# Performance work log

Measured on AMD Instinct MI355X. Metric: run time of the kernel, lower is better.

## Reference

```python
import jax, jax.numpy as jnp
import numpy as np

TAU = 2.0
V_TH = 0.5
BN_EPS = 1e-5
ALPHA = 2.0  # spikingjelly surrogate.ATan default

@jax.custom_vjp
def spike_fn(x):
    # Heaviside forward, ATan surrogate backward (defined for fwdbwd parity)
    return (x >= 0.0).astype(x.dtype)

def _spike_fwd(x):
    return spike_fn(x), x

def _spike_bwd(x, g):
    return (g * (ALPHA / 2.0) / (1.0 + (jnp.pi / 2.0 * ALPHA * x) ** 2),)

spike_fn.defvjp(_spike_fwd, _spike_bwd)

def lif_multistep(x_seq):
    # MultiStepLIFNode: v <- v + (x - v)/tau ; spike = H(v - v_th) ; hard reset v<-v*(1-sg(spike))
    def step(v, x_t):
        v = v + (x_t - v) / TAU
        s = spike_fn(v - V_TH)
        v = v * (1.0 - jax.lax.stop_gradient(s))  # detach_reset=True, v_reset=0
        return v, s
    v0 = jnp.zeros_like(x_seq[0])
    _, spikes = jax.lax.scan(step, v0, x_seq)
    return spikes

def setup_inputs() -> dict:
    key = jax.random.key(0)
    k1, k2, k3 = jax.random.split(key, 3)
    T, B, N, D = 4, 64, 256, 512
    x = jax.random.normal(k1, (T, B, N, D), jnp.float32)
    mx = jax.random.normal(k2, (N, B, T, D), jnp.float32)
    W = jax.random.normal(k3, (D, D), jnp.float32) / np.sqrt(D).astype(np.float32)
    gamma = jnp.ones((D,), jnp.float32)
    beta = jnp.zeros((D,), jnp.float32)
    return {"x": x, "mx": mx, "W": W, "gamma": gamma, "beta": beta}

def reference(x, mx, W, gamma, beta):
    # mx: [N,B,T,D] -> transpose(0,2) -> [T,B,N,D]
    mxt = jnp.transpose(mx, (2, 1, 0, 3))
    # Linear (no bias): [T,B,N,D] @ W^T
    h = jnp.einsum('tbnd,ed->tbne', mxt, W)
    # BatchNorm1d(D) in training mode: stats over (T*B, N) per channel D (biased var)
    mean = h.mean(axis=(0, 1, 2))
    var = h.var(axis=(0, 1, 2))
    hn = (h - mean) * jax.lax.rsqrt(var + BN_EPS) * gamma + beta
    # LIF recurrence over T
    s = lif_multistep(hn)  # [T,B,N,D] binary spikes
    return x * s
```

## Files before the change

### kernel.cpp

```cpp
#include <hip/hip_runtime.h>
#include <math.h>

namespace {
constexpr int TDIM = 4, BDIM = 64, NDIM = 256, DDIM = 512;
constexpr int MROWS = 65536;
constexpr long long BND = 8388608LL;
constexpr double BN_EPS = 1e-5;

constexpr int BM = 64, BNT = 128, BK = 32;
constexpr int APITCH = BK + 2;
constexpr int WPITCH = BNT + 4;
constexpr int LDS_BYTES = (BM * APITCH + BK * WPITCH) * 8;

constexpr int BM3 = 128, BN3 = 64, BK3 = 16;
constexpr int AP3 = BM3 + 1;
constexpr int WP3 = BN3 + 1;

constexpr int NSA = 6, NSW = 5;
constexpr long long APL = 33554432LL;
constexpr long long WPL = 262144LL;
constexpr int CH8 = 22528;
}

typedef double d4 __attribute__((ext_vector_type(4)));
typedef int i32x4 __attribute__((ext_vector_type(4)));
typedef int i32x16 __attribute__((ext_vector_type(16)));

#define GLOAD16(g, d) __builtin_amdgcn_global_load_lds( \
    (const __attribute__((address_space(1))) void*)(g), \
    (__attribute__((address_space(3))) void*)(d), 16, 0, 0)

__global__ void probe_k(double* __restrict__ rowmap)
{
    const int l = threadIdx.x;
    d4 z = {0.0, 0.0, 0.0, 0.0};
    d4 dr = __builtin_amdgcn_mfma_f64_16x16x4f64((double)(l & 15), 1.0, z, 0, 0, 0);
#pragma unroll
    for (int r = 0; r < 4; ++r)
        rowmap[l * 4 + r] = dr[r] * 0.25;
}

__global__ void probe8_k(double* __restrict__ irow8, double* __restrict__ icol8)
{
    const int l = threadIdx.x;
    i32x16 z;
#pragma unroll
    for (int r = 0; r < 16; ++r) z[r] = 0;
    const int mb = (l & 31) * 0x01010101;
    const int ob = 0x01010101;
    i32x4 am = {mb, mb, mb, mb};
    i32x4 a1 = {ob, ob, ob, ob};
    i32x16 d1 = __builtin_amdgcn_mfma_i32_32x32x32_i8(am, a1, z, 0, 0, 0);
#pragma unroll
    for (int r = 0; r < 16; ++r)
        irow8[l * 16 + r] = (double)d1[r] / 32.0;
    i32x16 d2 = __builtin_amdgcn_mfma_i32_32x32x32_i8(a1, am, z, 0, 0, 0);
    icol8[l] = (double)d2[0] / 32.0;
}

__global__ __launch_bounds__(256)
void slice_a_k(const float* __restrict__ src, char* __restrict__ dst)
{
    const int ri  = threadIdx.x & 63;
    const int ks0 = threadIdx.x >> 6;
    const long long row = (long long)blockIdx.x * 64 + ri;
#pragma unroll 1
    for (int it = 0; it < 8; ++it) {
        const int kseg = it * 4 + ks0;
        const float* sp = src + row * DDIM + kseg * 16;
        union { char c[16]; i32x4 v; } pk[NSA];
#pragma unroll
        for (int e = 0; e < 16; ++e) {
            const double V = (double)sp[e] * 4.0;
            const double u = rint(V);
            pk[0].c[e] = (char)(int)u;
            float r = (float)(V - u);
#pragma unroll
            for (int s = 1; s < NSA; ++s) {
                r *= 128.0f;
                const float uf = rintf(r);
                r -= uf;
                pk[s].c[e] = (char)(int)uf;
            }
        }
        const long long base = (long long)blockIdx.x * 32768 + kseg * 1024 + ri * 16;
#pragma unroll
        for (int s = 0; s < NSA; ++s)
            *(i32x4*)(dst + (long long)s * APL + base) = pk[s].v;
    }
}

__global__ __launch_bounds__(256)
void slice_w_k(const float* __restrict__ src, char* __restrict__ dst)
{
    const int cbk  = blockIdx.x >> 3;
    const int kgrp = blockIdx.x & 7;
    const int ci   = threadIdx.x & 63;
    const int kseg = kgrp * 4 + (threadIdx.x >> 6);
    const float* sp = src + (long long)(cbk * 64 + ci) * DDIM + kseg * 16;
    union { char c[16]; i32x4 v; } pk[NSW];
#pragma unroll
    for (int e = 0; e < 16; ++e) {
        const double V = (double)sp[e] * 256.0;
        const double u = rint(V);
        pk[0].c[e] = (char)(int)u;
        float r = (float)(V - u);
#pragma unroll
        for (int s = 1; s < NSW; ++s) {
            r *= 128.0f;
            const float uf = rintf(r);
            r -= uf;
            pk[s].c[e] = (char)(int)uf;
        }
    }
    const long long base = (long long)cbk * 32768 + kseg * 1024 + ci * 16;
#pragma unroll
    for (int s = 0; s < NSW; ++s)
        *(i32x4*)(dst + (long long)s * WPL + base) = pk[s].v;
}

template<int NW>
struct Stager {
    const char* gb[NW];
    int lo[NW];
    __device__ __forceinline__ void init(int w0, const char* Asl, const char* Wsl,
                                         long long aT, long long wT, int l)
    {
#pragma unroll
        for (int i = 0; i < NW; ++i) {
            const int idx = w0 + i;
            if (idx < 12) {
                gb[i] = Asl + (long long)(idx >> 1) * APL + aT
                      + (long long)(idx & 1) * 1024 + l * 16;
                lo[i] = (idx >> 1) * 2048 + (idx & 1) * 1024;
            } else {
                const int e = idx - 12;
                gb[i] = Wsl + (long long)(e >> 1) * WPL + wT
                      + (long long)(e & 1) * 1024 + l * 16;
                lo[i] = 12288 + (e >> 1) * 2048 + (e & 1) * 1024;
            }
        }
    }
    __device__ __forceinline__ void issue(char* buf, int ck)
    {
        const int go = ck * 2048;
#pragma unroll
        for (int i = 0; i < NW; ++i)
            GLOAD16(gb[i] + go, buf + lo[i]);
    }
};

template<int NW>
__device__ __forceinline__ void gemm8_loop(Stager<NW>& st, char* smb,
                                           i32x16 (&acc)[6], int roA, int roW,
                                           int c0)
{
#pragma unroll 2
    for (int c = 0; c < 16; ++c) {
        const char* bA = smb + (c & 1) * CH8;
        const char* bW = bA + 12288;
        i32x4 af[NSA], wf[NSW];
#pragma unroll
        for (int s = 0; s < NSA; ++s)
            af[s] = *(const i32x4*)(bA + s * 2048 + roA);
#pragma unroll
        for (int t = 0; t < NSW; ++t)
            wf[t] = *(const i32x4*)(bW + t * 2048 + roW);
#pragma unroll
        for (int s = 0; s < NSA; ++s)
#pragma unroll
            for (int t = 0; t < NSW; ++t)
                if (s + t <= 5)
                    acc[s + t] = __builtin_amdgcn_mfma_i32_32x32x32_i8(
                                     af[s], wf[t], acc[s + t], 0, 0, 0);
        if (c == 15) break;
        asm volatile("s_barrier" ::: "memory");
        if (c < 14) {
            st.issue(smb + (c & 1) * CH8, (c0 + c + 2) & 15);
            if constexpr (NW == 6)
                asm volatile("s_waitcnt vmcnt(6)" ::: "memory");
            else
                asm volatile("s_waitcnt vmcnt(5)" ::: "memory");
        } else {
            asm volatile("s_waitcnt vmcnt(0)" ::: "memory");
        }
        __builtin_amdgcn_sched_barrier(0);
        asm volatile("s_barrier" ::: "memory");
        __builtin_amdgcn_sched_barrier(0);
    }
}

__global__ __launch_bounds__(256, 3)
void gemm8_k(const char* __restrict__ Asl, const char* __restrict__ Wsl,
             double* __restrict__ hbuf, double* __restrict__ sums,
             const double* __restrict__ irow8, const double* __restrict__ icol8)
{
    __shared__ __align__(16) char sm[2][CH8];

    const int tid = threadIdx.x;
    const int bid = blockIdx.x;
    const int rb  = ((bid >> 6) << 3) | (bid & 7);
    const int cb  = (bid >> 3) & 7;

    const int c0 = (((bid >> 6) * 5) + ((bid & 7) * 3)) & 15;

    const int w  = tid >> 6;
    const int l  = tid & 63;
    const int wr = w >> 1;
    const int wc = w & 1;

    const long long aTile = (long long)rb * 32768;
    const long long wTile = (long long)cb * 32768;

    i32x16 acc[6];
#pragma unroll
    for (int g = 0; g < 6; ++g)
#pragma unroll
        for (int r = 0; r < 16; ++r) acc[g][r] = 0;

    const int roA = (l >> 5) * 1024 + (32 * wr + (l & 31)) * 16;
    const int roW = (l >> 5) * 1024 + (32 * wc + (l & 31)) * 16;

    char* smb = &sm[0][0];
    if (w < 2) {
        Stager<6> st;
        st.init(6 * w, Asl, Wsl, aTile, wTile, l);
        st.issue(smb, c0);
        st.issue(smb + CH8, (c0 + 1) & 15);
        asm volatile("s_waitcnt vmcnt(6)" ::: "memory");
        __builtin_amdgcn_sched_barrier(0);
        asm volatile("s_barrier" ::: "memory");
        __builtin_amdgcn_sched_barrier(0);
        gemm8_loop<6>(st, smb, acc, roA, roW, c0);
    } else {
        Stager<5> st;
        st.init(12 + 5 * (w - 2), Asl, Wsl, aTile, wTile, l);
        st.issue(smb, c0);
        st.issue(smb + CH8, (c0 + 1) & 15);
        asm volatile("s_waitcnt vmcnt(5)" ::: "memory");
        __builtin_amdgcn_sched_barrier(0);
        asm volatile("s_barrier" ::: "memory");
        __builtin_amdgcn_sched_barrier(0);
        gemm8_loop<5>(st, smb, acc, roA, roW, c0);
    }

    int irw[16];
#pragma unroll
    for (int r = 0; r < 16; ++r) irw[r] = (int)irow8[l * 16 + r];
    const int icl = (int)icol8[l];

    const double C7 = 1.0 / 128.0, CMB = 1.0 / 1024.0;
    double lsum = 0.0, lsq = 0.0;
    const int colg = cb * 64 + 32 * wc + icl;
    const int row0 = rb * 64 + 32 * wr;
#pragma unroll
    for (int r = 0; r < 16; ++r) {
        double t = (double)acc[5][r];
        t = fma(t, C7, (double)acc[4][r]);
        t = fma(t, C7, (double)acc[3][r]);
        t = fma(t, C7, (double)acc[2][r]);
        t = fma(t, C7, (double)acc[1][r]);
        t = fma(t, C7, (double)acc[0][r]);
        const double h = t * CMB;
        hbuf[(size_t)(row0 + irw[r]) * DDIM + colg] = h;
        lsum += h;
        lsq = fma(h, h, lsq);
    }

    __syncthreads();
    double* Ss = (double*)sm;
    const int ctr = wr * 2 + (l >> 5);
    const int cloc = 32 * wc + icl;
    Ss[cloc * 4 + ctr] = lsum;
    Ss[256 + cloc * 4 + ctr] = lsq;
    __syncthreads();
    if (tid < 64) {
        double s = 0.0, q = 0.0;
#pragma unroll
        for (int k = 0; k < 4; ++k) {
            s += Ss[tid * 4 + k];
            q += Ss[256 + tid * 4 + k];
        }
        atomicAdd(&sums[cb * 64 + tid], s);
        atomicAdd(&sums[512 + cb * 64 + tid], q);
    }
}

__global__ __launch_bounds__(256, 2)
void gemm3_k(const float* __restrict__ mx, const float* __restrict__ Wm,
             double* __restrict__ hbuf, double* __restrict__ sums,
             const double* __restrict__ rowmap)
{
    __shared__ double Atr[BK3 * AP3];
    __shared__ double Wt [BK3 * WP3];

    const int tid = threadIdx.x;
    const int bid = blockIdx.x;
    const int rb  = ((bid >> 6) << 3) | (bid & 7);
    const int cb  = (bid >> 3) & 7;
    const int row0 = rb * BM3;
    const int col0 = cb * BN3;

    const int w  = tid >> 6;
    const int l  = tid & 63;
    const int wr = w >> 1;
    const int wc = w & 1;
    const int lr = l & 15;
    const int kq = l >> 4;

    int irow[4];
#pragma unroll
    for (int r = 0; r < 4; ++r)
        irow[r] = (int)rowmap[l * 4 + r];

    const int arow = tid >> 1;
    const int af   = (tid & 1) * 8;
    const int wrow = tid >> 2;
    const int wf   = (tid & 3) * 4;
    const float* aSrc = mx + (size_t)(row0 + arow) * DDIM + af;
    const float* wSrc = Wm + (size_t)(col0 + wrow) * DDIM + wf;

    d4 acc[4][2];
#pragma unroll
    for (int i = 0; i < 4; ++i)
#pragma unroll
        for (int j = 0; j < 2; ++j) acc[i][j] = (d4){0.0, 0.0, 0.0, 0.0};

    float4 pa0 = *(const float4*)(aSrc + 0);
    float4 pa1 = *(const float4*)(aSrc + 4);
    float4 pw  = *(const float4*)(wSrc + 0);

    for (int kk = 0; kk < DDIM; kk += BK3) {
        __syncthreads();
        Atr[(af + 0) * AP3 + arow] = (double)pa0.x;
        Atr[(af + 1) * AP3 + arow] = (double)pa0.y;
        Atr[(af + 2) * AP3 + arow] = (double)pa0.z;
        Atr[(af + 3) * AP3 + arow] = (double)pa0.w;
        Atr[(af + 4) * AP3 + arow] = (double)pa1.x;
        Atr[(af + 5) * AP3 + arow] = (double)pa1.y;
        Atr[(af + 6) * AP3 + arow] = (double)pa1.z;
        Atr[(af + 7) * AP3 + arow] = (double)pa1.w;
        Wt[(wf + 0) * WP3 + wrow] = (double)pw.x;
        Wt[(wf + 1) * WP3 + wrow] = (double)pw.y;
        Wt[(wf + 2) * WP3 + wrow] = (double)pw.z;
        Wt[(wf + 3) * WP3 + wrow] = (double)pw.w;
        __syncthreads();

        if (kk + BK3 < DDIM) {
            pa0 = *(const float4*)(aSrc + kk + BK3 + 0);
            pa1 = *(const float4*)(aSrc + kk + BK3 + 4);
            pw  = *(const float4*)(wSrc + kk + BK3 + 0);
        }

#pragma unroll
        for (int ks = 0; ks < BK3 / 4; ++ks) {
            const int kabs = ks * 4 + kq;
            double a[4], b[2];
#pragma unroll
            for (int i = 0; i < 4; ++i)
                a[i] = Atr[kabs * AP3 + 64 * wr + 16 * i + lr];
#pragma unroll
            for (int j = 0; j < 2; ++j)
                b[j] = Wt[kabs * WP3 + 32 * wc + 16 * j + lr];
#pragma unroll
            for (int i = 0; i < 4; ++i)
#pragma unroll
                for (int j = 0; j < 2; ++j)
                    acc[i][j] = __builtin_amdgcn_mfma_f64_16x16x4f64(
                                    a[i], b[j], acc[i][j], 0, 0, 0);
        }
    }

#pragma unroll
    for (int i = 0; i < 4; ++i) {
#pragma unroll
        for (int j = 0; j < 2; ++j) {
            const size_t cbase = (size_t)col0 + 32 * wc + 16 * j + lr;
            const size_t rbase = (size_t)row0 + 64 * wr + 16 * i;
#pragma unroll
            for (int r = 0; r < 4; ++r)
                hbuf[(rbase + irow[r]) * DDIM + cbase] = acc[i][j][r];
        }
    }

    __syncthreads();
    double* Ssum = Atr;
    double* Ssq  = Atr + 512;
    const int ctr = wr * 4 + kq;
#pragma unroll
    for (int j = 0; j < 2; ++j) {
        const int cloc = 32 * wc + 16 * j + lr;
        double s = 0.0, q = 0.0;
#pragma unroll
        for (int i = 0; i < 4; ++i)
#pragma unroll
            for (int r = 0; r < 4; ++r) {
                const double v = acc[i][j][r];
                s += v;
                q = fma(v, v, q);
            }
        Ssum[cloc * 8 + ctr] = s;
        Ssq [cloc * 8 + ctr] = q;
    }
    __syncthreads();
    if (tid < 64) {
        double s = 0.0, q = 0.0;
#pragma unroll
        for (int c = 0; c < 8; ++c) {
            s += Ssum[tid * 8 + c];
            q += Ssq [tid * 8 + c];
        }
        atomicAdd(&sums[col0 + tid], s);
        atomicAdd(&sums[512 + col0 + tid], q);
    }
}

template<int MODE>
__global__ __launch_bounds__(256)
void gemm_k(const float* __restrict__ mx, const float* __restrict__ Wm,
            double* __restrict__ hbuf, double* __restrict__ sums,
            const double* __restrict__ scale, const double* __restrict__ shiftv,
            const float* __restrict__ x, float* __restrict__ out)
{
    __shared__ __align__(16) char smem[LDS_BYTES];
    double (*Ald)[APITCH] = reinterpret_cast<double(*)[APITCH]>(smem);
    double (*Wld)[WPITCH] = reinterpret_cast<double(*)[WPITCH]>(smem + (size_t)BM * APITCH * 8);

    const int tid  = threadIdx.x;
    const int rb   = blockIdx.x >> 2;
    const int cb   = blockIdx.x & 3;
    const int row0 = rb * BM;
    const int col0 = cb * BNT;

    const int arow = tid >> 2;
    const int ak   = (tid & 3) * 8;
    const int erow = tid >> 1;
    const int wk   = (tid & 1) * 16;

    const float* aSrc = mx + (size_t)(row0 + arow) * DDIM;
    const float* wSrc = Wm + (size_t)(col0 + erow) * DDIM;

    const int rg = tid >> 4;
    const int cg = tid & 15;

    double acc[4][8];
#pragma unroll
    for (int i = 0; i < 4; ++i)
#pragma unroll
        for (int j = 0; j < 8; ++j) acc[i][j] = 0.0;

    for (int kk = 0; kk < DDIM; kk += BK) {
        const float4 a0 = *(const float4*)(aSrc + kk + ak);
        const float4 a1 = *(const float4*)(aSrc + kk + ak + 4);
        const float4 w0 = *(const float4*)(wSrc + kk + wk);
        const float4 w1 = *(const float4*)(wSrc + kk + wk + 4);
        const float4 w2 = *(const float4*)(wSrc + kk + wk + 8);
        const float4 w3 = *(const float4*)(wSrc + kk + wk + 12);
        __syncthreads();
        Ald[arow][ak + 0] = (double)a0.x; Ald[arow][ak + 1] = (double)a0.y;
        Ald[arow][ak + 2] = (double)a0.z; Ald[arow][ak + 3] = (double)a0.w;
        Ald[arow][ak + 4] = (double)a1.x; Ald[arow][ak + 5] = (double)a1.y;
        Ald[arow][ak + 6] = (double)a1.z; Ald[arow][ak + 7] = (double)a1.w;
        const float wfv[16] = {w0.x, w0.y, w0.z, w0.w, w1.x, w1.y, w1.z, w1.w,
                               w2.x, w2.y, w2.z, w2.w, w3.x, w3.y, w3.z, w3.w};
#pragma unroll
        for (int q = 0; q < 16; ++q) Wld[wk + q][erow] = (double)wfv[q];
        __syncthreads();

#pragma unroll 4
        for (int d = 0; d < BK; ++d) {
            double a[4], wv[8];
#pragma unroll
            for (int i = 0; i < 4; ++i) a[i] = Ald[rg * 4 + i][d];
#pragma unroll
            for (int j = 0; j < 8; ++j) wv[j] = Wld[d][cg * 8 + j];
#pragma unroll
            for (int i = 0; i < 4; ++i)
#pragma unroll
                for (int j = 0; j < 8; ++j)
                    acc[i][j] = fma(a[i], wv[j], acc[i][j]);
        }
    }

    if (MODE <= 1) {
        __syncthreads();
        double* scr = reinterpret_cast<double*>(smem);
#pragma unroll
        for (int j = 0; j < 8; ++j) {
            const double s = acc[0][j] + acc[1][j] + acc[2][j] + acc[3][j];
            const double q = acc[0][j]*acc[0][j] + acc[1][j]*acc[1][j]
                           + acc[2][j]*acc[2][j] + acc[3][j]*acc[3][j];
            scr[(cg * 8 + j) * 16 + rg] = s;
            scr[2048 + (cg * 8 + j) * 16 + rg] = q;
        }
        __syncthreads();
        if (tid < 128) {
            double s = 0.0, q = 0.0;
#pragma unroll
            for (int r = 0; r < 16; ++r) {
                s += scr[tid * 16 + r];
                q += scr[2048 + tid * 16 + r];
            }
            atomicAdd(&sums[col0 + tid], s);
            atomicAdd(&sums[512 + col0 + tid], q);
        }
    }

    if (MODE == 2) {
        const int p  = rb * 16 + rg;
        const int nn = p >> 6;
        const int bb = p & 63;
#pragma unroll
        for (int j = 0; j < 8; ++j) {
            const int e = col0 + cg * 8 + j;
            const double sc = scale[e];
            const double sh = shiftv[e];
            const size_t basex = (size_t)bb * (NDIM * DDIM) + (size_t)nn * DDIM + e;
            double v = 0.0;
#pragma unroll
            for (int t = 0; t < 4; ++t) {
                const double hn = fma(acc[t][j], sc, sh);
                v = v + (hn - v) / 2.0;
                const bool s = (v - 0.5) >= 0.0;
                const size_t xi = (size_t)t * BND + basex;
                out[xi] = s ? x[xi] : 0.0f;
                if (s) v = 0.0;
            }
        }
    }
}

__global__ void zero_k(double* sums)
{
    const int i = blockIdx.x * 256 + threadIdx.x;
    if (i < 1024) sums[i] = 0.0;
}

__global__ void stat_k(const double* __restrict__ sums,
                       const float* __restrict__ gamma, const float* __restrict__ beta,
                       double* __restrict__ scale, double* __restrict__ shiftv)
{
    const int e = blockIdx.x * 256 + threadIdx.x;
    if (e < 512) {
        const double mean = sums[e] * (1.0 / 65536.0);
        const double msq  = sums[512 + e] * (1.0 / 65536.0);
        const double var  = msq - mean * mean;
        const double inv  = 1.0 / sqrt(var + BN_EPS);
        const double g    = (double)gamma[e] * inv;
        scale[e]  = g;
        shiftv[e] = (double)beta[e] - mean * g;
    }
}

__global__ __launch_bounds__(256)
void lifh_k(const double* __restrict__ hbuf, const double* __restrict__ scale,
            const double* __restrict__ shiftv, const float* __restrict__ x,
            float* __restrict__ out)
{
    const size_t i = (size_t)blockIdx.x * 256 + threadIdx.x;
    const int e2 = (int)(i & 255) * 2;
    const size_t p = i >> 8;
    const int nn = (int)(p >> 6);
    const int bb = (int)(p & 63);
    const double2 sc = *(const double2*)&scale[e2];
    const double2 sh = *(const double2*)&shiftv[e2];
    const double* hp = hbuf + p * 2048 + e2;
    const size_t basex = (size_t)bb * (NDIM * DDIM) + (size_t)nn * DDIM + e2;
    double v0 = 0.0, v1 = 0.0;
#pragma unroll
    for (int t = 0; t < 4; ++t) {
        const double2 h2 = *(const double2*)(hp + (size_t)t * 512);
        const double hn0 = fma(h2.x, sc.x, sh.x);
        const double hn1 = fma(h2.y, sc.y, sh.y);
        v0 = v0 + (hn0 - v0) / 2.0;
        v1 = v1 + (hn1 - v1) / 2.0;
        const bool s0 = (v0 - 0.5) >= 0.0;
        const bool s1 = (v1 - 0.5) >= 0.0;
        const size_t xi = (size_t)t * BND + basex;
        const float2 xv = *(const float2*)(x + xi);
        float2 ov;
        ov.x = s0 ? xv.x : 0.0f;
        ov.y = s1 ? xv.y : 0.0f;
        *(float2*)(out + xi) = ov;
        if (s0) v0 = 0.0;
        if (s1) v1 = 0.0;
    }
}

extern "C" void kernel_launch(void* const* d_in, const int* in_sizes, int n_in,
                              void* d_out, int out_size, void* d_ws, size_t ws_size,
                              hipStream_t stream)
{
    const float* x     = (const float*)d_in[0];
    const float* mx    = (const float*)d_in[1];
    const float* Wm    = (const float*)d_in[2];
    const float* gamma = (const float*)d_in[3];
    const float* beta  = (const float*)d_in[4];
    float* out = (float*)d_out;

    char* ws = (char*)d_ws;
    double* sums   = (double*)ws;
    double* scale  = (double*)(ws + 8192);
    double* shiftv = scale + 512;
    double* rowmap = (double*)(ws + 16384);
    double* irow8  = (double*)(ws + 18432);
    double* icol8  = (double*)(ws + 26624);
    double* hbuf   = (double*)(ws + 32768);

    const size_t HBSZ   = (size_t)MROWS * DDIM * 8;
    const size_t OFF_AS = 32768 + HBSZ;
    const size_t ASSZ   = (size_t)NSA * APL;
    const size_t OFF_WS = OFF_AS + ASSZ;
    const size_t WSSZ   = (size_t)NSW * WPL;
    const size_t need8  = OFF_WS + WSSZ;
    const size_t need_h = 32768 + HBSZ;

    hipLaunchKernelGGL(zero_k, dim3(4), dim3(256), 0, stream, sums);

    if (ws_size >= need8) {
        char* Asl = ws + OFF_AS;
        char* Wsl = ws + OFF_WS;
        hipLaunchKernelGGL(probe8_k, dim3(1), dim3(64), 0, stream, irow8, icol8);
        hipLaunchKernelGGL(slice_a_k, dim3(1024), dim3(256), 0, stream, mx, Asl);
        hipLaunchKernelGGL(slice_w_k, dim3(64), dim3(256), 0, stream, Wm, Wsl);
        hipLaunchKernelGGL(gemm8_k, dim3(8192), dim3(256), 0, stream,
                           Asl, Wsl, hbuf, sums, irow8, icol8);
        hipLaunchKernelGGL(stat_k, dim3(2), dim3(256), 0, stream,
                           sums, gamma, beta, scale, shiftv);
        hipLaunchKernelGGL(lifh_k, dim3(16384), dim3(256), 0, stream,
                           hbuf, scale, shiftv, x, out);
    } else if (ws_size >= need_h) {
        hipLaunchKernelGGL(probe_k, dim3(1), dim3(64), 0, stream, rowmap);
        hipLaunchKernelGGL(gemm3_k, dim3(4096), dim3(256), 0, stream,
                           mx, Wm, hbuf, sums, rowmap);
        hipLaunchKernelGGL(stat_k, dim3(2), dim3(256), 0, stream,
                           sums, gamma, beta, scale, shiftv);
        hipLaunchKernelGGL(lifh_k, dim3(16384), dim3(256), 0, stream,
                           hbuf, scale, shiftv, x, out);
    } else {
        hipLaunchKernelGGL((gemm_k<0>), dim3(4096), dim3(256), 0, stream,
                           mx, Wm, nullptr, sums, nullptr, nullptr, nullptr, nullptr);
        hipLaunchKernelGGL(stat_k, dim3(2), dim3(256), 0, stream,
                           sums, gamma, beta, scale, shiftv);
        hipLaunchKernelGGL((gemm_k<2>), dim3(4096), dim3(256), 0, stream,
                           mx, Wm, nullptr, nullptr, scale, shiftv, x, out);
    }
}
```

Before: 472.9 us.

## Restructure int8 GEMM tiles: per-wave private A staging and register-held W fragments

Reworks the int8 sliced GEMM kernel so each block covers 128 rows by 32 columns, and each wave owns a private 32-row A slice. That slice is double-buffered in LDS through direct global-to-LDS loads, while the W fragments go straight into registers. Because no wave reads another wave's LDS data, the two block-wide barriers per K-chunk are dropped. In exchange, W fragments are reloaded from global memory by every wave and there is more register pressure, so launch bounds drop from 3 to 2 blocks per CU. The grid mapping and the BN statistics reduction change to match the new tile shape.

```diff
diff --git a/kernel.cpp b/kernel.cpp
--- a/kernel.cpp
+++ b/kernel.cpp
@@ -19,7 +19,6 @@
 constexpr int NSA = 6, NSW = 5;
 constexpr long long APL = 33554432LL;
 constexpr long long WPL = 262144LL;
-constexpr int CH8 = 22528;
 }
 
 typedef double d4 __attribute__((ext_vector_type(4)));
@@ -119,129 +118,85 @@
         *(i32x4*)(dst + (long long)s * WPL + base) = pk[s].v;
 }
 
-template<int NW>
-struct Stager {
-    const char* gb[NW];
-    int lo[NW];
-    __device__ __forceinline__ void init(int w0, const char* Asl, const char* Wsl,
-                                         long long aT, long long wT, int l)
-    {
-#pragma unroll
-        for (int i = 0; i < NW; ++i) {
-            const int idx = w0 + i;
-            if (idx < 12) {
-                gb[i] = Asl + (long long)(idx >> 1) * APL + aT
-                      + (long long)(idx & 1) * 1024 + l * 16;
-                lo[i] = (idx >> 1) * 2048 + (idx & 1) * 1024;
-            } else {
-                const int e = idx - 12;
-                gb[i] = Wsl + (long long)(e >> 1) * WPL + wT
-                      + (long long)(e & 1) * 1024 + l * 16;
-                lo[i] = 12288 + (e >> 1) * 2048 + (e & 1) * 1024;
-            }
-        }
-    }
-    __device__ __forceinline__ void issue(char* buf, int ck)
-    {
-        const int go = ck * 2048;
-#pragma unroll
-        for (int i = 0; i < NW; ++i)
-            GLOAD16(gb[i] + go, buf + lo[i]);
-    }
-};
-
-template<int NW>
-__device__ __forceinline__ void gemm8_loop(Stager<NW>& st, char* smb,
-                                           i32x16 (&acc)[6], int roA, int roW,
-                                           int c0)
-{
-#pragma unroll 2
-    for (int c = 0; c < 16; ++c) {
-        const char* bA = smb + (c & 1) * CH8;
-        const char* bW = bA + 12288;
-        i32x4 af[NSA], wf[NSW];
-#pragma unroll
-        for (int s = 0; s < NSA; ++s)
-            af[s] = *(const i32x4*)(bA + s * 2048 + roA);
-#pragma unroll
-        for (int t = 0; t < NSW; ++t)
-            wf[t] = *(const i32x4*)(bW + t * 2048 + roW);
-#pragma unroll
-        for (int s = 0; s < NSA; ++s)
-#pragma unroll
-            for (int t = 0; t < NSW; ++t)
-                if (s + t <= 5)
-                    acc[s + t] = __builtin_amdgcn_mfma_i32_32x32x32_i8(
-                                     af[s], wf[t], acc[s + t], 0, 0, 0);
-        if (c == 15) break;
-        asm volatile("s_barrier" ::: "memory");
-        if (c < 14) {
-            st.issue(smb + (c & 1) * CH8, (c0 + c + 2) & 15);
-            if constexpr (NW == 6)
-                asm volatile("s_waitcnt vmcnt(6)" ::: "memory");
-            else
-                asm volatile("s_waitcnt vmcnt(5)" ::: "memory");
-        } else {
-            asm volatile("s_waitcnt vmcnt(0)" ::: "memory");
-        }
-        __builtin_amdgcn_sched_barrier(0);
-        asm volatile("s_barrier" ::: "memory");
-        __builtin_amdgcn_sched_barrier(0);
-    }
-}
-
-__global__ __launch_bounds__(256, 3)
+__global__ __launch_bounds__(256, 2)
 void gemm8_k(const char* __restrict__ Asl, const char* __restrict__ Wsl,
              double* __restrict__ hbuf, double* __restrict__ sums,
              const double* __restrict__ irow8, const double* __restrict__ icol8)
 {
-    __shared__ __align__(16) char sm[2][CH8];
+    __shared__ __align__(16) char sm[49152];
 
     const int tid = threadIdx.x;
     const int bid = blockIdx.x;
-    const int rb  = ((bid >> 6) << 3) | (bid & 7);
-    const int cb  = (bid >> 3) & 7;
-
-    const int c0 = (((bid >> 6) * 5) + ((bid & 7) * 3)) & 15;
-
-    const int w  = tid >> 6;
-    const int l  = tid & 63;
-    const int wr = w >> 1;
-    const int wc = w & 1;
-
-    const long long aTile = (long long)rb * 32768;
-    const long long wTile = (long long)cb * 32768;
+    const int g   = bid >> 7;
+    const int cbb = (bid >> 3) & 15;
+    const int xcd = bid & 7;
+    const int rb  = g * 8 + xcd;
+    const int c0  = ((g * 5) + (cbb * 3)) & 15;
+
+    const int w = tid >> 6;
+    const int l = tid & 63;
+
+    const long long aBase = ((long long)(rb * 2 + (w >> 1))) * 32768
+                          + (long long)(l >> 5) * 1024
+                          + (long long)(32 * (w & 1) + (l & 31)) * 16;
+    const long long wBase = ((long long)(cbb >> 1)) * 32768
+                          + (long long)(l >> 5) * 1024
+                          + (long long)(32 * (cbb & 1) + (l & 31)) * 16;
+
+    char* myA = sm + w * 12288;
 
     i32x16 acc[6];
 #pragma unroll
-    for (int g = 0; g < 6; ++g)
-#pragma unroll
-        for (int r = 0; r < 16; ++r) acc[g][r] = 0;
-
-    const int roA = (l >> 5) * 1024 + (32 * wr + (l & 31)) * 16;
-    const int roW = (l >> 5) * 1024 + (32 * wc + (l & 31)) * 16;
-
-    char* smb = &sm[0][0];
-    if (w < 2) {
-        Stager<6> st;
-        st.init(6 * w, Asl, Wsl, aTile, wTile, l);
-        st.issue(smb, c0);
-        st.issue(smb + CH8, (c0 + 1) & 15);
-        asm volatile("s_waitcnt vmcnt(6)" ::: "memory");
+    for (int gg = 0; gg < 6; ++gg)
+#pragma unroll
+        for (int r = 0; r < 16; ++r) acc[gg][r] = 0;
+
+    i32x4 wreg[2][5];
+
+    {
+        const long long wo = wBase + (long long)c0 * 2048;
+#pragma unroll
+        for (int t = 0; t < 5; ++t)
+            wreg[0][t] = *(const i32x4*)(Wsl + (long long)t * WPL + wo);
+        const long long ao = aBase + (long long)c0 * 2048;
+#pragma unroll
+        for (int s = 0; s < 6; ++s)
+            GLOAD16(Asl + (long long)s * APL + ao, myA + s * 1024);
+    }
+
+#pragma unroll 2
+    for (int c = 0; c < 16; ++c) {
+        const int cur = c & 1;
+        if (c < 15) {
+            const int ck = (c0 + c + 1) & 15;
+            const long long wo = wBase + (long long)ck * 2048;
+#pragma unroll
+            for (int t = 0; t < 5; ++t)
+                wreg[cur ^ 1][t] = *(const i32x4*)(Wsl + (long long)t * WPL + wo);
+            const long long ao = aBase + (long long)ck * 2048;
+#pragma unroll
+            for (int s = 0; s < 6; ++s)
+                GLOAD16(Asl + (long long)s * APL + ao,
+                        myA + (cur ^ 1) * 6144 + s * 1024);
+            __builtin_amdgcn_sched_barrier(0);
+            asm volatile("s_waitcnt vmcnt(11)" ::: "memory");
+        } else {
+            __builtin_amdgcn_sched_barrier(0);
+            asm volatile("s_waitcnt vmcnt(0)" ::: "memory");
+        }
         __builtin_amdgcn_sched_barrier(0);
-        asm volatile("s_barrier" ::: "memory");
-        __builtin_amdgcn_sched_barrier(0);
-        gemm8_loop<6>(st, smb, acc, roA, roW, c0);
-    } else {
-        Stager<5> st;
-        st.init(12 + 5 * (w - 2), Asl, Wsl, aTile, wTile, l);
-        st.issue(smb, c0);
-        st.issue(smb + CH8, (c0 + 1) & 15);
-        asm volatile("s_waitcnt vmcnt(5)" ::: "memory");
-        __builtin_amdgcn_sched_barrier(0);
-        asm volatile("s_barrier" ::: "memory");
-        __builtin_amdgcn_sched_barrier(0);
-        gemm8_loop<5>(st, smb, acc, roA, roW, c0);
+
+        i32x4 af[6];
+#pragma unroll
+        for (int s = 0; s < 6; ++s)
+            af[s] = *(const i32x4*)(myA + cur * 6144 + s * 1024 + l * 16);
+#pragma unroll
+        for (int s = 0; s < 6; ++s)
+#pragma unroll
+            for (int t = 0; t < 5; ++t)
+                if (s + t <= 5)
+                    acc[s + t] = __builtin_amdgcn_mfma_i32_32x32x32_i8(
+                                     af[s], wreg[cur][t], acc[s + t], 0, 0, 0);
     }
 
     int irw[16];
@@ -251,8 +206,8 @@
 
     const double C7 = 1.0 / 128.0, CMB = 1.0 / 1024.0;
     double lsum = 0.0, lsq = 0.0;
-    const int colg = cb * 64 + 32 * wc + icl;
-    const int row0 = rb * 64 + 32 * wr;
+    const int colg = cbb * 32 + icl;
+    const int row0 = rb * 128 + 32 * w;
 #pragma unroll
     for (int r = 0; r < 16; ++r) {
         double t = (double)acc[5][r];
@@ -269,20 +224,19 @@
 
     __syncthreads();
     double* Ss = (double*)sm;
-    const int ctr = wr * 2 + (l >> 5);
-    const int cloc = 32 * wc + icl;
-    Ss[cloc * 4 + ctr] = lsum;
-    Ss[256 + cloc * 4 + ctr] = lsq;
+    const int ctr = w * 2 + (l >> 5);
+    Ss[icl * 8 + ctr] = lsum;
+    Ss[256 + icl * 8 + ctr] = lsq;
     __syncthreads();
-    if (tid < 64) {
+    if (tid < 32) {
         double s = 0.0, q = 0.0;
 #pragma unroll
-        for (int k = 0; k < 4; ++k) {
-            s += Ss[tid * 4 + k];
-            q += Ss[256 + tid * 4 + k];
-        }
-        atomicAdd(&sums[cb * 64 + tid], s);
-        atomicAdd(&sums[512 + cb * 64 + tid], q);
+        for (int k = 0; k < 8; ++k) {
+            s += Ss[tid * 8 + k];
+            q += Ss[256 + tid * 8 + k];
+        }
+        atomicAdd(&sums[cbb * 32 + tid], s);
+        atomicAdd(&sums[512 + cbb * 32 + tid], q);
     }
 }
 
```

New measurement: 546.6 us. 15.6% more time.
